# Kernel optimization log

Measured on AMD Instinct MI355X. Metric: run time of the kernel, lower is better.

The kernel has to match this reference:

```python
import jax, jax.numpy as jnp
import numpy as np

B, SEQ, S, DIM_IN, DIM_K, DIM_V = 4, 2048, 128, 512, 64, 64
L = SEQ + 2 * S
NEG = -1e30  # stand-in for log(0) in the tril mask (finite for stable vjp)


def _layernorm(x, g, b, eps=1e-5):
    m = jnp.mean(x, axis=-1, keepdims=True)
    v = jnp.var(x, axis=-1, keepdims=True)
    return (x - m) / jnp.sqrt(v + eps) * g + b


def setup_inputs() -> dict:
    key = jax.random.key(0)
    ks = jax.random.split(key, 18)
    w = lambda k, shape, s=0.02: (jax.random.normal(k, shape, jnp.float32) * s)
    inp = {
        "x": jax.random.normal(ks[0], (B, L, DIM_IN), jnp.float32),
        "Wq": w(ks[1], (DIM_IN, DIM_K)),
        "Wk": w(ks[2], (DIM_IN, DIM_K)),
        "Wv": w(ks[3], (DIM_IN, DIM_V)),
        "Wq_s": w(ks[4], (DIM_IN, DIM_K)),
        "Wk_s": w(ks[5], (DIM_IN, DIM_K)),
        "Wv_s": w(ks[6], (DIM_IN, DIM_V)),
        "Wq_e": w(ks[7], (DIM_IN, DIM_K)),
        "Wk_e": w(ks[8], (DIM_IN, DIM_K)),
        "Wv_e": w(ks[9], (DIM_IN, DIM_V)),
        "ln_g": jnp.ones((DIM_IN,), jnp.float32),
        "ln_b": jnp.zeros((DIM_IN,), jnp.float32),
        "ln_s_g": jnp.ones((DIM_IN,), jnp.float32),
        "ln_s_b": jnp.zeros((DIM_IN,), jnp.float32),
        "ln_e_g": jnp.ones((DIM_IN,), jnp.float32),
        "ln_e_b": jnp.zeros((DIM_IN,), jnp.float32),
        "cope_emb": jax.random.normal(ks[10], (DIM_K, S), jnp.float32),
        "offset": 0,
    }
    return inp


def reference(x, Wq, Wk, Wv, Wq_s, Wk_s, Wv_s, Wq_e, Wk_e, Wv_e,
              ln_g, ln_b, ln_s_g, ln_s_b, ln_e_g, ln_e_b, cope_emb, offset):
    # extract_state: first/last state_len tokens
    xs, xm, xe = x[:, :S], x[:, S:L - S], x[:, -S:]
    xm = _layernorm(xm, ln_g, ln_b)
    xs = _layernorm(xs, ln_s_g, ln_s_b)
    xe = _layernorm(xe, ln_e_g, ln_e_b)

    q, k, v = xm @ Wq, xm @ Wk, xm @ Wv          # (B, SEQ, dk/dv)
    q_s, k_s, v_s = xs @ Wq_s, xs @ Wk_s, xs @ Wv_s
    q_e, k_e, v_e = xe @ Wq_e, xe @ Wk_e, xe @ Wv_e

    # CoPE bias over the non-state block
    logits = jnp.einsum('bqd,bkd->bqk', q, k)    # (B, SEQ, SEQ)
    gates = jax.nn.sigmoid(logits)
    pos = jnp.flip(jnp.cumsum(jnp.flip(gates, -1), axis=-1), -1)
    pos = jnp.minimum(pos, jnp.float32(S - 1))
    pos_ceil = jnp.ceil(pos).astype(jnp.int32)
    pos_floor = jnp.floor(pos).astype(jnp.int32)
    logits_int = jnp.einsum('bqd,dk->bqk', q, cope_emb)  # (B, SEQ, S)
    logits_c = jnp.take_along_axis(logits_int, pos_ceil, axis=-1)
    logits_f = jnp.take_along_axis(logits_int, pos_floor, axis=-1)
    wfrac = pos - pos_floor.astype(pos.dtype)
    bias = logits_c * wfrac + logits_f * (1.0 - wfrac)   # (B, SEQ, SEQ)

    q_full = jnp.concatenate([q_s, q, q_e], axis=1)      # (B, L, dk)
    k_full = jnp.concatenate([k_s, k, k_e], axis=1)
    v_full = jnp.concatenate([v_s, v, v_e], axis=1)

    # explicit tril log-mask bias with CoPE injected in the middle block
    tri = jnp.tril(jnp.ones((L, L), dtype=bool))
    attn_bias = jnp.where(tri, 0.0, NEG).astype(jnp.float32)
    attn_bias = jnp.broadcast_to(attn_bias, (B, L, L))
    attn_bias = attn_bias.at[:, S:L - S, S:L - S].add(bias)

    scale = 1.0 / jnp.sqrt(jnp.float32(DIM_K))
    scores = jnp.einsum('bqd,bkd->bqk', q_full, k_full) * scale + attn_bias
    att = jax.nn.softmax(scores, axis=-1)
    return jnp.einsum('bqk,bkd->bqd', att, v_full)       # (B, L, dv)
```

## Files before the change

kernel.cpp:

```cpp
#include <hip/hip_runtime.h>
#include <math.h>

#define B_    4
#define SEQ_  2048
#define S_    128
#define L_    2304
#define DIN   512
#define DK    64
#define NEGINF (-1e30f)
#define SCALE 0.125f
#define NCOLS 2176
#define NMID  8192
#define NEDGE 1024
#define LE    2304
#define PROWS 4352
#define PEPITCH 4608

typedef _Float16 f16;
typedef __attribute__((ext_vector_type(8))) _Float16 half8;
typedef __attribute__((ext_vector_type(4))) float f32x4;

union U4 { uint4 u; f16 h[8]; };

__global__ __launch_bounds__(256) void k_ln(
    const float* __restrict__ x,
    const float* __restrict__ g0, const float* __restrict__ b0,
    const float* __restrict__ gs, const float* __restrict__ bs,
    const float* __restrict__ ge, const float* __restrict__ be,
    f16* __restrict__ xh, f16* __restrict__ xl)
{
    const int wave = threadIdx.x >> 6, lane = threadIdx.x & 63;
    const int row  = blockIdx.x * 4 + wave;
    const float4* xr = (const float4*)(x + (size_t)row * DIN);
    float4 v0 = xr[lane], v1 = xr[lane + 64];
    float s  = v0.x + v0.y + v0.z + v0.w + v1.x + v1.y + v1.z + v1.w;
    float s2 = v0.x*v0.x + v0.y*v0.y + v0.z*v0.z + v0.w*v0.w
             + v1.x*v1.x + v1.y*v1.y + v1.z*v1.z + v1.w*v1.w;
    #pragma unroll
    for (int m = 1; m < 64; m <<= 1) { s += __shfl_xor(s, m); s2 += __shfl_xor(s2, m); }
    float mean = s * (1.f / DIN);
    float var  = s2 * (1.f / DIN) - mean * mean;
    float rstd = rsqrtf(var + 1e-5f);

    const int r = row % L_;
    const float *gg, *bb;
    if (r < S_)            { gg = gs; bb = bs; }
    else if (r >= L_ - S_) { gg = ge; bb = be; }
    else                   { gg = g0; bb = b0; }
    float4 ga = ((const float4*)gg)[lane], gb = ((const float4*)gg)[lane + 64];
    float4 ba = ((const float4*)bb)[lane], bb4 = ((const float4*)bb)[lane + 64];

    float n0[4], n1[4];
    n0[0] = (v0.x - mean) * rstd * ga.x + ba.x;
    n0[1] = (v0.y - mean) * rstd * ga.y + ba.y;
    n0[2] = (v0.z - mean) * rstd * ga.z + ba.z;
    n0[3] = (v0.w - mean) * rstd * ga.w + ba.w;
    n1[0] = (v1.x - mean) * rstd * gb.x + bb4.x;
    n1[1] = (v1.y - mean) * rstd * gb.y + bb4.y;
    n1[2] = (v1.z - mean) * rstd * gb.z + bb4.z;
    n1[3] = (v1.w - mean) * rstd * gb.w + bb4.w;

    union { uint2 u; f16 h[4]; } h0, h1, l0, l1;
    #pragma unroll
    for (int i = 0; i < 4; ++i) {
        h0.h[i] = (f16)n0[i]; l0.h[i] = (f16)(n0[i] - (float)h0.h[i]);
        h1.h[i] = (f16)n1[i]; l1.h[i] = (f16)(n1[i] - (float)h1.h[i]);
    }
    f16* ph = xh + (size_t)row * DIN;
    f16* pl = xl + (size_t)row * DIN;
    *(uint2*)(ph + 4 * lane)       = h0.u;
    *(uint2*)(ph + 256 + 4 * lane) = h1.u;
    *(uint2*)(pl + 4 * lane)       = l0.u;
    *(uint2*)(pl + 256 + 4 * lane) = l1.u;
}

__global__ __launch_bounds__(256) void k_proj(
    const f16* __restrict__ xh, const f16* __restrict__ xl,
    const float* __restrict__ Wq,  const float* __restrict__ Wk,  const float* __restrict__ Wv,
    const float* __restrict__ Wqs, const float* __restrict__ Wks, const float* __restrict__ Wvs,
    const float* __restrict__ Wqe, const float* __restrict__ Wke, const float* __restrict__ Wve,
    float* __restrict__ qf, float* __restrict__ kf, float* __restrict__ vf,
    f16* __restrict__ qsp, f16* __restrict__ ksp, f16* __restrict__ vhT)
{
    __shared__ f16 As[64 * 136];
    __shared__ f16 Bs[64 * 136];
    const int tid  = threadIdx.x;
    const int row0 = blockIdx.x * 64;
    const int rseq = row0 % L_;
    const int seg  = (rseq < S_) ? 0 : (rseq >= L_ - S_) ? 2 : 1;
    const int m    = blockIdx.y;
    const float* W;
    float* outf;
    if (m == 0)      { W = (seg == 0) ? Wqs : (seg == 2) ? Wqe : Wq; outf = qf; }
    else if (m == 1) { W = (seg == 0) ? Wks : (seg == 2) ? Wke : Wk; outf = kf; }
    else             { W = (seg == 0) ? Wvs : (seg == 2) ? Wve : Wv; outf = vf; }

    const int w = tid >> 6, lane = tid & 63;
    const int cl = lane & 15, quad = lane >> 4;
    const int r0 = 32 * (w >> 1), c0 = 32 * (w & 1);

    f32x4 acc[2][2];
    #pragma unroll
    for (int i = 0; i < 2; ++i)
        #pragma unroll
        for (int j = 0; j < 2; ++j) acc[i][j] = 0.f;

    for (int kc = 0; kc < DIN; kc += 64) {
        __syncthreads();
        #pragma unroll
        for (int i = 0; i < 2; ++i) {
            int g = tid + 256 * i;
            int r = g >> 3, c = g & 7;
            *(uint4*)(As + r * 136 + c * 8) =
                *(const uint4*)(xh + (size_t)(row0 + r) * DIN + kc + c * 8);
            *(uint4*)(As + r * 136 + 64 + c * 8) =
                *(const uint4*)(xl + (size_t)(row0 + r) * DIN + kc + c * 8);
        }
        #pragma unroll
        for (int i = 0; i < 4; ++i) {
            int g = tid + 256 * i;
            int k = g >> 4, c4 = g & 15;
            float4 wv = ((const float4*)W)[(size_t)(kc + k) * 16 + c4];
            f16 h0 = (f16)wv.x, h1 = (f16)wv.y, h2 = (f16)wv.z, h3 = (f16)wv.w;
            Bs[(c4 * 4 + 0) * 136 + k] = h0;
            Bs[(c4 * 4 + 1) * 136 + k] = h1;
            Bs[(c4 * 4 + 2) * 136 + k] = h2;
            Bs[(c4 * 4 + 3) * 136 + k] = h3;
            Bs[(c4 * 4 + 0) * 136 + 64 + k] = (f16)(wv.x - (float)h0);
            Bs[(c4 * 4 + 1) * 136 + 64 + k] = (f16)(wv.y - (float)h1);
            Bs[(c4 * 4 + 2) * 136 + 64 + k] = (f16)(wv.z - (float)h2);
            Bs[(c4 * 4 + 3) * 136 + 64 + k] = (f16)(wv.w - (float)h3);
// ... 28 lines not shown
    }

    const int bI = row0 / L_;
    const int rb = row0 - bI * L_;
    f16* sp = (m == 0) ? qsp : ksp;
    #pragma unroll
    for (int rs = 0; rs < 2; ++rs)
        #pragma unroll
        for (int cs = 0; cs < 2; ++cs)
            #pragma unroll
            for (int r = 0; r < 4; ++r) {
                int lrow = r0 + 16 * rs + quad * 4 + r;
                int col  = c0 + 16 * cs + cl;
                float v  = acc[rs][cs][r];
                size_t grow = (size_t)(row0 + lrow);
                outf[grow * DK + col] = v;
                if (m < 2) {
                    f16 hv = (f16)v;
                    sp[grow * 128 + col]      = hv;
                    sp[grow * 128 + 64 + col] = (f16)(v - (float)hv);
                } else {
                    vhT[(size_t)(bI * 64 + col) * L_ + rb + lrow] = (f16)v;
                }
            }
}

__global__ __launch_bounds__(256) void k_dots(
    const f16* __restrict__ qsp, const f16* __restrict__ ksp,
    float* __restrict__ D, float* __restrict__ G)
{
    __shared__ f16 Qs[128 * 136];
    __shared__ f16 Ks[64 * 136];
    const int tid  = threadIdx.x;
    const int gr0  = blockIdx.x * 128;
    const int by   = blockIdx.y;
    const int col0 = by * 64;
    const int b    = gr0 >> 11;
    const int q0   = gr0 & 2047;
    const size_t qrow0 = (size_t)b * L_ + S_ + q0;
    const size_t krow0 = (size_t)b * L_ + col0;

    #pragma unroll
    for (int i = 0; i < 8; ++i) {
        int g = tid + 256 * i;
        int r = g >> 4, c = g & 15;
        *(uint4*)(Qs + r * 136 + c * 8) = *(const uint4*)(qsp + (qrow0 + r) * 128 + c * 8);
    }
    #pragma unroll
    for (int i = 0; i < 4; ++i) {
        int g = tid + 256 * i;
        int r = g >> 4, c = g & 15;
        *(uint4*)(Ks + r * 136 + c * 8) = *(const uint4*)(ksp + (krow0 + r) * 128 + c * 8);
    }
    __syncthreads();

// ... 19 lines not shown
        for (int c = 0; c < 4; ++c) {
            const f16* base = Ks + (16 * c + cl) * 136 + h * 32 + quad * 8;
            bh[c] = *(const half8*)(base);
            bl[c] = *(const half8*)(base + 64);
        }
        #pragma unroll
        for (int rs = 0; rs < 2; ++rs)
            #pragma unroll
            for (int c = 0; c < 4; ++c) {
                acc[rs][c] = __builtin_amdgcn_mfma_f32_16x16x32_f16(ah[rs], bh[c], acc[rs][c], 0, 0, 0);
                acc[rs][c] = __builtin_amdgcn_mfma_f32_16x16x32_f16(ah[rs], bl[c], acc[rs][c], 0, 0, 0);
                acc[rs][c] = __builtin_amdgcn_mfma_f32_16x16x32_f16(al[rs], bh[c], acc[rs][c], 0, 0, 0);
            }
    }

    const bool writeD = (by < 2) || ((by - 2) <= (q0 >> 6) + 1);
    if (writeD) {
        #pragma unroll
        for (int rs = 0; rs < 2; ++rs)
            #pragma unroll
            for (int c = 0; c < 4; ++c)
                #pragma unroll
                for (int r = 0; r < 4; ++r) {
                    int mrow = gr0 + 32 * w + 16 * rs + quad * 4 + r;
                    int n    = col0 + 16 * c + cl;
                    D[(size_t)mrow * NCOLS + n] = acc[rs][c][r];
                }
    }
    if (by >= 2) {
        const int chm = by - 2;
        #pragma unroll
        for (int rs = 0; rs < 2; ++rs)
            #pragma unroll
            for (int r = 0; r < 4; ++r) {
                float s = 0.f;
                #pragma unroll
                for (int c = 0; c < 4; ++c)
                    s += 1.f / (1.f + __expf(-acc[rs][c][r]));
                #pragma unroll
                for (int off = 1; off < 16; off <<= 1) s += __shfl_xor(s, off);
                if (cl == 0)
                    G[(size_t)(gr0 + 32 * w + 16 * rs + quad * 4 + r) * 32 + chm] = s;
            }
    }
}

__global__ __launch_bounds__(256) void k_scan(
    const float* __restrict__ qf, const float* __restrict__ cope,
    const float* __restrict__ G, float* __restrict__ D)
{
    __shared__ float qv[DK];
    __shared__ float li[128];
    __shared__ float red[256];
    __shared__ float wtot[4];
    __shared__ float Gs[32];
    const int tid = threadIdx.x;
    const int gr  = blockIdx.x;
    const int b   = gr >> 11;
    const int q   = gr & 2047;
    const size_t grow = (size_t)b * L_ + S_ + q;
    const int qlim = (q & ~63) + 64;

    if (tid < 16) ((float4*)qv)[tid] = ((const float4*)qf)[grow * 16 + tid];
    if (tid >= 16 && tid < 24) ((float4*)Gs)[tid - 16] = ((const float4*)G)[(size_t)gr * 8 + tid - 16];
    __syncthreads();
    if (tid < 128) {
        float a = 0.f;
        #pragma unroll
        for (int d = 0; d < DK; ++d) a += qv[d] * cope[d * S_ + tid];
        li[tid] = a;
    }

    const float* Dr = D + (size_t)gr * NCOLS;
    const int j0 = tid * 8;
    float dot[8], gte[8];
    float csum = 0.f;
    if (j0 < qlim) {
        *(float4*)&dot[0] = *(const float4*)(Dr + 128 + j0);
        *(float4*)&dot[4] = *(const float4*)(Dr + 128 + j0 + 4);
        #pragma unroll
        for (int jj = 0; jj < 8; ++jj) {
            gte[jj] = 1.f / (1.f + __expf(-dot[jj]));
            csum += gte[jj];
        }
    } else {
        #pragma unroll
        for (int jj = 0; jj < 8; ++jj) { dot[jj] = 0.f; gte[jj] = 0.f; }
    }
    float sv = (tid < 128) ? Dr[tid] * SCALE : NEGINF;

    const int lane = tid & 63, wid = tid >> 6;
    float inc = csum;
    #pragma unroll
    for (int off = 1; off < 64; off <<= 1) {
        float u = __shfl_down(inc, off, 64);
        if (lane + off < 64) inc += u;
    }
    if (lane == 0) wtot[wid] = inc;
    __syncthreads();
    float wsuf = 0.f;
    #pragma unroll
    for (int w = 0; w < 4; ++w) if (w > wid) wsuf += wtot[w];
    float tail = 0.f;
    for (int c = (q >> 6) + 1; c < 32; ++c) tail += Gs[c];
    float run = inc - csum + wsuf + tail;

    float p8[8];
    #pragma unroll
    for (int jj = 7; jj >= 0; --jj) {
        run += gte[jj];
        float pos = fminf(run, (float)(S_ - 1));
        float pfl = floorf(pos);
        int ic  = (int)ceilf(pos);
        int ifl = (int)pfl;
        float w = pos - pfl;
        float bias = li[ic] * w + li[ifl] * (1.f - w);
        p8[jj] = (j0 + jj <= q) ? dot[jj] * SCALE + bias : NEGINF;
    }

    float mx = sv;
    #pragma unroll
    for (int jj = 0; jj < 8; ++jj) mx = fmaxf(mx, p8[jj]);
    red[tid] = mx;
    __syncthreads();
    for (int off = 128; off > 0; off >>= 1) {
        if (tid < off) red[tid] = fmaxf(red[tid], red[tid + off]);
        __syncthreads();
    }
    mx = red[0];
    __syncthreads();

    float lsum = 0.f;
    float e8[8];
    #pragma unroll
    for (int jj = 0; jj < 8; ++jj) {
        e8[jj] = __expf(p8[jj] - mx);
        lsum += e8[jj];
    }
    float es = 0.f;
    if (tid < 128) { es = __expf(sv - mx); lsum += es; }
    red[tid] = lsum;
    __syncthreads();
    for (int off = 128; off > 0; off >>= 1) {
        if (tid < off) red[tid] += red[tid + off];
        __syncthreads();
    }
    float inv = 1.f / red[0];

    f16* pb = (f16*)D + (size_t)gr * PROWS;
    if (j0 < qlim) {
        U4 o;
        #pragma unroll
        for (int jj = 0; jj < 8; ++jj) o.h[jj] = (f16)(e8[jj] * inv);
        *(uint4*)(pb + 128 + j0) = o.u;
    }
    if (tid < 128) pb[tid] = (f16)(es * inv);
}

__global__ __launch_bounds__(256) void k_pv(
    const f16* __restrict__ Pb, const f16* __restrict__ vhT,
    float* __restrict__ Opart)
{
    __shared__ f16 Ps[64 * 72];
    __shared__ f16 Vt[64 * 72];
    const int tid = threadIdx.x;
    const int gr0 = blockIdx.x * 64;
    const int ks  = blockIdx.y;
    const int b   = gr0 >> 11, q0 = gr0 & 2047;
    const int cmax  = (191 + q0) >> 6;
    const int c_beg = ks * 9;
    int c_end = c_beg + 9;
    if (c_end > 34) c_end = 34;
    if (c_end > cmax + 1) c_end = cmax + 1;

    const int w = tid >> 6, lane = tid & 63;
    const int cl = lane & 15, quad = lane >> 4;
    f32x4 acc[4];
    #pragma unroll
    for (int c = 0; c < 4; ++c) acc[c] = 0.f;

    for (int ch = c_beg; ch < c_end; ++ch) {
        __syncthreads();
        #pragma unroll
        for (int i = 0; i < 2; ++i) {
            int g = tid + 256 * i;
            int r = g >> 3, c = g & 7;
            *(uint4*)(Ps + r * 72 + c * 8) =
                *(const uint4*)(Pb + (size_t)(gr0 + r) * PROWS + ch * 64 + c * 8);
            *(uint4*)(Vt + r * 72 + c * 8) =
                *(const uint4*)(vhT + (size_t)(b * 64 + r) * L_ + ch * 64 + c * 8);
        }
        __syncthreads();
        #pragma unroll
        for (int h = 0; h < 2; ++h) {
            half8 a = *(const half8*)(Ps + (16 * w + cl) * 72 + h * 32 + quad * 8);
            #pragma unroll
            for (int c = 0; c < 4; ++c) {
                half8 bv = *(const half8*)(Vt + (16 * c + cl) * 72 + h * 32 + quad * 8);
                acc[c] = __builtin_amdgcn_mfma_f32_16x16x32_f16(a, bv, acc[c], 0, 0, 0);
            }
        }
    }
    #pragma unroll
    for (int c = 0; c < 4; ++c)
        #pragma unroll
        for (int r = 0; r < 4; ++r) {
            int mrow = gr0 + 16 * w + quad * 4 + r;
            int n    = 16 * c + cl;
            Opart[((size_t)ks * NMID + mrow) * DK + n] = acc[c][r];
        }
}

__global__ __launch_bounds__(256) void k_merge(
    const float* __restrict__ Opart, float* __restrict__ out)
{
    const int e  = blockIdx.x * 256 + threadIdx.x;
    const int gr = e >> 6, c = e & 63;
    const int b  = gr >> 11, q = gr & 2047;
    const int NP = NMID * DK;
    float s = Opart[e] + Opart[e + NP] + Opart[e + 2 * NP] + Opart[e + 3 * NP];
    out[((size_t)b * L_ + S_ + q) * DK + c] = s;
}

__global__ __launch_bounds__(256) void k_dots_edge(
    const f16* __restrict__ qsp, const f16* __restrict__ ksp,
    float* __restrict__ De)
{
    const int bx   = blockIdx.x;
    const int b    = bx >> 1;
    const int half = bx & 1;
    const int by   = blockIdx.y;
    if (half == 0 && by > 1) return;

    __shared__ f16 Qs[128 * 136];
    __shared__ f16 Ks[64 * 136];
    const int tid = threadIdx.x;
    const int er0 = bx * 128;
    const size_t qrow0 = (size_t)b * L_ + (half ? 2176 : 0);
    const size_t krow0 = (size_t)b * L_ + by * 64;

    #pragma unroll
    for (int i = 0; i < 8; ++i) {
        int g = tid + 256 * i;
        int r = g >> 4, c = g & 15;
        *(uint4*)(Qs + r * 136 + c * 8) = *(const uint4*)(qsp + (qrow0 + r) * 128 + c * 8);
    }
    #pragma unroll
    for (int i = 0; i < 4; ++i) {
        int g = tid + 256 * i;
        int r = g >> 4, c = g & 15;
        *(uint4*)(Ks + r * 136 + c * 8) = *(const uint4*)(ksp + (krow0 + r) * 128 + c * 8);
    }
    __syncthreads();

    const int w = tid >> 6, lane = tid & 63;
    const int cl = lane & 15, quad = lane >> 4;

    f32x4 acc[2][4];
    #pragma unroll
    for (int i = 0; i < 2; ++i)
        #pragma unroll
        for (int j = 0; j < 4; ++j) acc[i][j] = 0.f;

    #pragma unroll
    for (int h = 0; h < 2; ++h) {
        half8 ah[2], al[2], bh[4], bl[4];
        #pragma unroll
        for (int rs = 0; rs < 2; ++rs) {
            const f16* base = Qs + (32 * w + 16 * rs + cl) * 136 + h * 32 + quad * 8;
            ah[rs] = *(const half8*)(base);
            al[rs] = *(const half8*)(base + 64);
        }
        #pragma unroll
        for (int c = 0; c < 4; ++c) {
            const f16* base = Ks + (16 * c + cl) * 136 + h * 32 + quad * 8;
            bh[c] = *(const half8*)(base);
            bl[c] = *(const half8*)(base + 64);
        }
        #pragma unroll
        for (int rs = 0; rs < 2; ++rs)
            #pragma unroll
            for (int c = 0; c < 4; ++c) {
                acc[rs][c] = __builtin_amdgcn_mfma_f32_16x16x32_f16(ah[rs], bh[c], acc[rs][c], 0, 0, 0);
                acc[rs][c] = __builtin_amdgcn_mfma_f32_16x16x32_f16(ah[rs], bl[c], acc[rs][c], 0, 0, 0);
                acc[rs][c] = __builtin_amdgcn_mfma_f32_16x16x32_f16(al[rs], bh[c], acc[rs][c], 0, 0, 0);
            }
    }

    #pragma unroll
    for (int rs = 0; rs < 2; ++rs)
        #pragma unroll
        for (int c = 0; c < 4; ++c)
            #pragma unroll
            for (int r = 0; r < 4; ++r) {
                int erow = er0 + 32 * w + 16 * rs + quad * 4 + r;
                int n    = by * 64 + 16 * c + cl;
                De[(size_t)erow * LE + n] = acc[rs][c][r];
            }
}

__global__ __launch_bounds__(256) void k_soft_edge(float* __restrict__ De)
{
    __shared__ float red[256];
    const int tid = threadIdx.x;
    const int er  = blockIdx.x;
    const int r   = er & 255;
    const int Q   = (r < 128) ? r : (2048 + r);
    const size_t rowoff = (size_t)er * LE;

    float v[9];
    #pragma unroll
    for (int i = 0; i < 9; ++i) {
        int j = tid + 256 * i;
        float d = De[rowoff + j];
        v[i] = (j <= Q) ? d * SCALE : NEGINF;
    }
    float mx = v[0];
    #pragma unroll
    for (int i = 1; i < 9; ++i) mx = fmaxf(mx, v[i]);
    red[tid] = mx;
    __syncthreads();
    for (int off = 128; off > 0; off >>= 1) {
        if (tid < off) red[tid] = fmaxf(red[tid], red[tid + off]);
        __syncthreads();
    }
    mx = red[0];
    __syncthreads();

    float lsum = 0.f;
    #pragma unroll
    for (int i = 0; i < 9; ++i) {
        v[i] = __expf(v[i] - mx);
        lsum += v[i];
    }
    red[tid] = lsum;
    __syncthreads();
    for (int off = 128; off > 0; off >>= 1) {
        if (tid < off) red[tid] += red[tid + off];
        __syncthreads();
    }
    float inv = 1.f / red[0];
    f16* pe = (f16*)De + (size_t)er * PEPITCH;
    #pragma unroll
    for (int i = 0; i < 9; ++i)
        pe[tid + 256 * i] = (f16)(v[i] * inv);
}

__global__ __launch_bounds__(256) void k_pv_edge(
    const f16* __restrict__ Pe, const f16* __restrict__ vhT,
    float* __restrict__ Oe)
{
    __shared__ f16 Ps[64 * 72];
    __shared__ f16 Vt[64 * 72];
    const int tid = threadIdx.x;
    const int er0 = blockIdx.x * 64;
    const int ks  = blockIdx.y;
    const int b   = er0 >> 8, r0 = er0 & 255;
    const int Qmax = (r0 < 128) ? (r0 + 63) : (2048 + r0 + 63);
    const int cmax = Qmax >> 6;
    const int c_beg = ks * 5;
    int c_end = c_beg + 5;
    if (c_end > 36) c_end = 36;
    if (c_end > cmax + 1) c_end = cmax + 1;

    const int w = tid >> 6, lane = tid & 63;
    const int cl = lane & 15, quad = lane >> 4;
    f32x4 acc[4];
    #pragma unroll
    for (int c = 0; c < 4; ++c) acc[c] = 0.f;

    for (int ch = c_beg; ch < c_end; ++ch) {
        __syncthreads();
        #pragma unroll
        for (int i = 0; i < 2; ++i) {
            int g = tid + 256 * i;
            int r = g >> 3, c = g & 7;
            *(uint4*)(Ps + r * 72 + c * 8) =
                *(const uint4*)(Pe + (size_t)(er0 + r) * PEPITCH + ch * 64 + c * 8);
            *(uint4*)(Vt + r * 72 + c * 8) =
                *(const uint4*)(vhT + (size_t)(b * 64 + r) * L_ + ch * 64 + c * 8);
        }
        __syncthreads();
        #pragma unroll
        for (int h = 0; h < 2; ++h) {
            half8 a = *(const half8*)(Ps + (16 * w + cl) * 72 + h * 32 + quad * 8);
            #pragma unroll
            for (int c = 0; c < 4; ++c) {
                half8 bv = *(const half8*)(Vt + (16 * c + cl) * 72 + h * 32 + quad * 8);
                acc[c] = __builtin_amdgcn_mfma_f32_16x16x32_f16(a, bv, acc[c], 0, 0, 0);
            }
        }
    }
    #pragma unroll
    for (int c = 0; c < 4; ++c)
        #pragma unroll
        for (int r = 0; r < 4; ++r) {
            int erow = er0 + 16 * w + quad * 4 + r;
            int n    = 16 * c + cl;
            Oe[((size_t)ks * NEDGE + erow) * DK + n] = acc[c][r];
        }
}

__global__ __launch_bounds__(256) void k_merge_edge(
    const float* __restrict__ Oe, float* __restrict__ out)
{
    const int e  = blockIdx.x * 256 + threadIdx.x;
    const int er = e >> 6, c = e & 63;
    const int b  = er >> 8, r = er & 255;
    const int gQ = (r < 128) ? r : (2048 + r);
    const int NP = NEDGE * DK;
    float s = 0.f;
    #pragma unroll
    for (int i = 0; i < 8; ++i) s += Oe[e + i * NP];
    out[((size_t)b * L_ + gQ) * DK + c] = s;
}

extern "C" void kernel_launch(void* const* d_in, const int* in_sizes, int n_in,
                              void* d_out, int out_size, void* d_ws, size_t ws_size,
                              hipStream_t stream)
{
    const float* x    = (const float*)d_in[0];
    const float* Wq   = (const float*)d_in[1];
    const float* Wk   = (const float*)d_in[2];
    const float* Wv   = (const float*)d_in[3];
    const float* Wqs  = (const float*)d_in[4];
    const float* Wks  = (const float*)d_in[5];
    const float* Wvs  = (const float*)d_in[6];
    const float* Wqe  = (const float*)d_in[7];
    const float* Wke  = (const float*)d_in[8];
    const float* Wve  = (const float*)d_in[9];
    const float* g0   = (const float*)d_in[10];
    const float* b0   = (const float*)d_in[11];
    const float* gs   = (const float*)d_in[12];
    const float* bs   = (const float*)d_in[13];
    const float* ge   = (const float*)d_in[14];
    const float* be   = (const float*)d_in[15];
    const float* cope = (const float*)d_in[16];

    const size_t NR = (size_t)B_ * L_;
    float* ws = (float*)d_ws;
    float* qf    = ws;
    float* kf    = qf + NR * DK;
    float* vf    = kf + NR * DK;
    float* Opart = vf + NR * DK;
    float* G     = Opart + (size_t)4 * NMID * DK;
    f16*   qsp   = (f16*)(G + (size_t)NMID * 32);
    f16*   ksp   = qsp + NR * 128;
    f16*   vhT   = ksp + NR * 128;
    float* D     = (float*)(vhT + NR * DK);
    f16*   xh    = (f16*)D;
    f16*   xl    = xh + NR * DIN;
    float* De    = D;
    float* Oe    = Opart;
    float* out   = (float*)d_out;

    k_ln  <<<L_ * B_ / 4, 256, 0, stream>>>(x, g0, b0, gs, bs, ge, be, xh, xl);
    k_proj<<<dim3(144, 3), 256, 0, stream>>>(xh, xl, Wq, Wk, Wv, Wqs, Wks, Wvs,
                                             Wqe, Wke, Wve, qf, kf, vf,
                                             qsp, ksp, vhT);
    k_dots<<<dim3(NMID / 128, 34), 256, 0, stream>>>(qsp, ksp, D, G);
    k_scan<<<NMID, 256, 0, stream>>>(qf, cope, G, D);
    k_pv  <<<dim3(NMID / 64, 4), 256, 0, stream>>>((const f16*)D, vhT, Opart);
    k_merge<<<NMID * DK / 256, 256, 0, stream>>>(Opart, out);
    k_dots_edge<<<dim3(8, 36), 256, 0, stream>>>(qsp, ksp, De);
    k_soft_edge<<<NEDGE, 256, 0, stream>>>(De);
    k_pv_edge<<<dim3(NEDGE / 64, 8), 256, 0, stream>>>((const f16*)De, vhT, Oe);
    k_merge_edge<<<NEDGE * DK / 256, 256, 0, stream>>>(Oe, out);
}
```

Baseline: 223.2 us.

## Fuse layernorm into projection and merge edge-path kernels into main-path kernels

Layernorm is folded into the projection kernel: per-row statistics are computed in shared memory and the hi/lo f16 split happens while A tiles are staged, which removes the separate LN pass and its f16 round-trip through memory. The edge-row dots, softmax, PV and merge kernels are combined with their middle-block counterparts by widening grids and branching on block index, so ten launches become five. The fp32 q/k/v outputs are dropped, and CoPE logits are now rebuilt from the split f16 q. The cost is some extra reads of x and gamma/beta per projection block, plus idle early-exit blocks in the combined dots grid.

```diff
diff --git a/kernel.cpp b/kernel.cpp
--- a/kernel.cpp
+++ b/kernel.cpp
@@ -22,78 +22,49 @@
 
 union U4 { uint4 u; f16 h[8]; };
 
-__global__ __launch_bounds__(256) void k_ln(
+__global__ __launch_bounds__(256) void k_proj(
     const float* __restrict__ x,
+    const float* __restrict__ Wq,  const float* __restrict__ Wk,  const float* __restrict__ Wv,
+    const float* __restrict__ Wqs, const float* __restrict__ Wks, const float* __restrict__ Wvs,
+    const float* __restrict__ Wqe, const float* __restrict__ Wke, const float* __restrict__ Wve,
     const float* __restrict__ g0, const float* __restrict__ b0,
     const float* __restrict__ gs, const float* __restrict__ bs,
     const float* __restrict__ ge, const float* __restrict__ be,
-    f16* __restrict__ xh, f16* __restrict__ xl)
-{
-    const int wave = threadIdx.x >> 6, lane = threadIdx.x & 63;
-    const int row  = blockIdx.x * 4 + wave;
-    const float4* xr = (const float4*)(x + (size_t)row * DIN);
-    float4 v0 = xr[lane], v1 = xr[lane + 64];
-    float s  = v0.x + v0.y + v0.z + v0.w + v1.x + v1.y + v1.z + v1.w;
-    float s2 = v0.x*v0.x + v0.y*v0.y + v0.z*v0.z + v0.w*v0.w
-             + v1.x*v1.x + v1.y*v1.y + v1.z*v1.z + v1.w*v1.w;
-    #pragma unroll
-    for (int m = 1; m < 64; m <<= 1) { s += __shfl_xor(s, m); s2 += __shfl_xor(s2, m); }
-    float mean = s * (1.f / DIN);
-    float var  = s2 * (1.f / DIN) - mean * mean;
-    float rstd = rsqrtf(var + 1e-5f);
-
-    const int r = row % L_;
-    const float *gg, *bb;
-    if (r < S_)            { gg = gs; bb = bs; }
-    else if (r >= L_ - S_) { gg = ge; bb = be; }
-    else                   { gg = g0; bb = b0; }
-    float4 ga = ((const float4*)gg)[lane], gb = ((const float4*)gg)[lane + 64];
-    float4 ba = ((const float4*)bb)[lane], bb4 = ((const float4*)bb)[lane + 64];
-
-    float n0[4], n1[4];
-    n0[0] = (v0.x - mean) * rstd * ga.x + ba.x;
-    n0[1] = (v0.y - mean) * rstd * ga.y + ba.y;
-    n0[2] = (v0.z - mean) * rstd * ga.z + ba.z;
-    n0[3] = (v0.w - mean) * rstd * ga.w + ba.w;
-    n1[0] = (v1.x - mean) * rstd * gb.x + bb4.x;
-    n1[1] = (v1.y - mean) * rstd * gb.y + bb4.y;
-    n1[2] = (v1.z - mean) * rstd * gb.z + bb4.z;
-    n1[3] = (v1.w - mean) * rstd * gb.w + bb4.w;
-
-    union { uint2 u; f16 h[4]; } h0, h1, l0, l1;
-    #pragma unroll
-    for (int i = 0; i < 4; ++i) {
-        h0.h[i] = (f16)n0[i]; l0.h[i] = (f16)(n0[i] - (float)h0.h[i]);
-        h1.h[i] = (f16)n1[i]; l1.h[i] = (f16)(n1[i] - (float)h1.h[i]);
-    }
-    f16* ph = xh + (size_t)row * DIN;
-    f16* pl = xl + (size_t)row * DIN;
-    *(uint2*)(ph + 4 * lane)       = h0.u;
-    *(uint2*)(ph + 256 + 4 * lane) = h1.u;
-    *(uint2*)(pl + 4 * lane)       = l0.u;
-    *(uint2*)(pl + 256 + 4 * lane) = l1.u;
-}
-
-__global__ __launch_bounds__(256) void k_proj(
-    const f16* __restrict__ xh, const f16* __restrict__ xl,
-    const float* __restrict__ Wq,  const float* __restrict__ Wk,  const float* __restrict__ Wv,
-    const float* __restrict__ Wqs, const float* __restrict__ Wks, const float* __restrict__ Wvs,
-    const float* __restrict__ Wqe, const float* __restrict__ Wke, const float* __restrict__ Wve,
-    float* __restrict__ qf, float* __restrict__ kf, float* __restrict__ vf,
     f16* __restrict__ qsp, f16* __restrict__ ksp, f16* __restrict__ vhT)
 {
     __shared__ f16 As[64 * 136];
     __shared__ f16 Bs[64 * 136];
+    __shared__ float mean_s[64], rstd_s[64];
     const int tid  = threadIdx.x;
     const int row0 = blockIdx.x * 64;
     const int rseq = row0 % L_;
     const int seg  = (rseq < S_) ? 0 : (rseq >= L_ - S_) ? 2 : 1;
     const int m    = blockIdx.y;
     const float* W;
-    float* outf;
-    if (m == 0)      { W = (seg == 0) ? Wqs : (seg == 2) ? Wqe : Wq; outf = qf; }
-    else if (m == 1) { W = (seg == 0) ? Wks : (seg == 2) ? Wke : Wk; outf = kf; }
-    else             { W = (seg == 0) ? Wvs : (seg == 2) ? Wve : Wv; outf = vf; }
+    if (m == 0)      W = (seg == 0) ? Wqs : (seg == 2) ? Wqe : Wq;
+    else if (m == 1) W = (seg == 0) ? Wks : (seg == 2) ? Wke : Wk;
+    else             W = (seg == 0) ? Wvs : (seg == 2) ? Wve : Wv;
+    const float* gg = (seg == 0) ? gs : (seg == 2) ? ge : g0;
+    const float* bb = (seg == 0) ? bs : (seg == 2) ? be : b0;
+
+    {
+        const int rr = tid >> 2, qq = tid & 3;
+        const float4* xr = (const float4*)(x + (size_t)(row0 + rr) * DIN) + qq * 32;
+        float s = 0.f, s2 = 0.f;
+        #pragma unroll
+        for (int i = 0; i < 32; ++i) {
+            float4 v = xr[i];
+            s  += v.x + v.y + v.z + v.w;
+            s2 += v.x * v.x + v.y * v.y + v.z * v.z + v.w * v.w;
+        }
+        s  += __shfl_xor(s, 1);  s  += __shfl_xor(s, 2);
+        s2 += __shfl_xor(s2, 1); s2 += __shfl_xor(s2, 2);
+        if (qq == 0) {
+            float mean = s * (1.f / DIN);
+            mean_s[rr] = mean;
+            rstd_s[rr] = rsqrtf(s2 * (1.f / DIN) - mean * mean + 1e-5f);
+        }
+    }
 
     const int w = tid >> 6, lane = tid & 63;
     const int cl = lane & 15, quad = lane >> 4;
@@ -110,11 +81,32 @@
         #pragma unroll
         for (int i = 0; i < 2; ++i) {
             int g = tid + 256 * i;
-            int r = g >> 3, c = g & 7;
-            *(uint4*)(As + r * 136 + c * 8) =
-                *(const uint4*)(xh + (size_t)(row0 + r) * DIN + kc + c * 8);
-            *(uint4*)(As + r * 136 + 64 + c * 8) =
-                *(const uint4*)(xl + (size_t)(row0 + r) * DIN + kc + c * 8);
+            int r = g >> 3, c8 = g & 7;
+            const float* xp = x + (size_t)(row0 + r) * DIN + kc + c8 * 8;
+            float4 a0 = *(const float4*)xp;
+            float4 a1 = *(const float4*)(xp + 4);
+            float4 gA = *(const float4*)(gg + kc + c8 * 8);
+            float4 gB = *(const float4*)(gg + kc + c8 * 8 + 4);
+            float4 bA = *(const float4*)(bb + kc + c8 * 8);
+            float4 bB = *(const float4*)(bb + kc + c8 * 8 + 4);
+            float mean = mean_s[r], rstd = rstd_s[r];
+            float n[8];
+            n[0] = (a0.x - mean) * rstd * gA.x + bA.x;
+            n[1] = (a0.y - mean) * rstd * gA.y + bA.y;
+            n[2] = (a0.z - mean) * rstd * gA.z + bA.z;
+            n[3] = (a0.w - mean) * rstd * gA.w + bA.w;
+            n[4] = (a1.x - mean) * rstd * gB.x + bB.x;
+            n[5] = (a1.y - mean) * rstd * gB.y + bB.y;
+            n[6] = (a1.z - mean) * rstd * gB.z + bB.z;
+            n[7] = (a1.w - mean) * rstd * gB.w + bB.w;
+            U4 hi, lo;
+            #pragma unroll
+            for (int j = 0; j < 8; ++j) {
+                hi.h[j] = (f16)n[j];
+                lo.h[j] = (f16)(n[j] - (float)hi.h[j]);
+            }
+            *(uint4*)(As + r * 136 + c8 * 8)      = hi.u;
+            *(uint4*)(As + r * 136 + 64 + c8 * 8) = lo.u;
         }
         #pragma unroll
         for (int i = 0; i < 4; ++i) {
@@ -173,7 +165,6 @@
                 int col  = c0 + 16 * cs + cl;
                 float v  = acc[rs][cs][r];
                 size_t grow = (size_t)(row0 + lrow);
-                outf[grow * DK + col] = v;
                 if (m < 2) {
                     f16 hv = (f16)v;
                     sp[grow * 128 + col]      = hv;
@@ -186,18 +177,30 @@
 
 __global__ __launch_bounds__(256) void k_dots(
     const f16* __restrict__ qsp, const f16* __restrict__ ksp,
-    float* __restrict__ D, float* __restrict__ G)
+    float* __restrict__ D, float* __restrict__ G, float* __restrict__ De)
 {
+    const int bx = blockIdx.x, by = blockIdx.y;
+    const bool edge = (bx >= 64);
+    int b, q0 = 0;
+    size_t qrow0;
+    if (!edge) {
+        if (by >= 34) return;
+        b = bx >> 4;
+        q0 = (bx * 128) & 2047;
+        qrow0 = (size_t)b * L_ + S_ + q0;
+    } else {
+        int ex = bx - 64;
+        b = ex >> 1;
+        int half = ex & 1;
+        if (half == 0 && by > 1) return;
+        qrow0 = (size_t)b * L_ + (half ? 2176 : 0);
+    }
+    const int col0 = by * 64;
+    const size_t krow0 = (size_t)b * L_ + col0;
+
     __shared__ f16 Qs[128 * 136];
     __shared__ f16 Ks[64 * 136];
-    const int tid  = threadIdx.x;
-    const int gr0  = blockIdx.x * 128;
-    const int by   = blockIdx.y;
-    const int col0 = by * 64;
-    const int b    = gr0 >> 11;
-    const int q0   = gr0 & 2047;
-    const size_t qrow0 = (size_t)b * L_ + S_ + q0;
-    const size_t krow0 = (size_t)b * L_ + col0;
+    const int tid = threadIdx.x;
 
     #pragma unroll
     for (int i = 0; i < 8; ++i) {
@@ -247,163 +250,236 @@
             }
     }
 
-    const bool writeD = (by < 2) || ((by - 2) <= (q0 >> 6) + 1);
-    if (writeD) {
+    if (!edge) {
+        const int gr0 = bx * 128;
+        const bool writeD = (by < 2) || ((by - 2) <= (q0 >> 6) + 1);
+        if (writeD) {
+            #pragma unroll
+            for (int rs = 0; rs < 2; ++rs)
+                #pragma unroll
+                for (int c = 0; c < 4; ++c)
+                    #pragma unroll
+                    for (int r = 0; r < 4; ++r) {
+                        int mrow = gr0 + 32 * w + 16 * rs + quad * 4 + r;
+                        int n    = col0 + 16 * c + cl;
+                        D[(size_t)mrow * NCOLS + n] = acc[rs][c][r];
+                    }
+        }
+        if (by >= 2) {
+            const int chm = by - 2;
+            #pragma unroll
+            for (int rs = 0; rs < 2; ++rs)
+                #pragma unroll
+                for (int r = 0; r < 4; ++r) {
+                    float s = 0.f;
+                    #pragma unroll
+                    for (int c = 0; c < 4; ++c)
+                        s += 1.f / (1.f + __expf(-acc[rs][c][r]));
+                    #pragma unroll
+                    for (int off = 1; off < 16; off <<= 1) s += __shfl_xor(s, off);
+                    if (cl == 0)
+                        G[(size_t)(gr0 + 32 * w + 16 * rs + quad * 4 + r) * 32 + chm] = s;
+                }
+        }
+    } else {
+        const int er0 = (bx - 64) * 128;
         #pragma unroll
         for (int rs = 0; rs < 2; ++rs)
             #pragma unroll
             for (int c = 0; c < 4; ++c)
                 #pragma unroll
                 for (int r = 0; r < 4; ++r) {
-                    int mrow = gr0 + 32 * w + 16 * rs + quad * 4 + r;
+                    int erow = er0 + 32 * w + 16 * rs + quad * 4 + r;
                     int n    = col0 + 16 * c + cl;
-                    D[(size_t)mrow * NCOLS + n] = acc[rs][c][r];
+                    De[(size_t)erow * LE + n] = acc[rs][c][r];
                 }
     }
-    if (by >= 2) {
-        const int chm = by - 2;
-        #pragma unroll
-        for (int rs = 0; rs < 2; ++rs)
-            #pragma unroll
-            for (int r = 0; r < 4; ++r) {
-                float s = 0.f;
-                #pragma unroll
-                for (int c = 0; c < 4; ++c)
-                    s += 1.f / (1.f + __expf(-acc[rs][c][r]));
-                #pragma unroll
-                for (int off = 1; off < 16; off <<= 1) s += __shfl_xor(s, off);
-                if (cl == 0)
-                    G[(size_t)(gr0 + 32 * w + 16 * rs + quad * 4 + r) * 32 + chm] = s;
-            }
-    }
 }
 
 __global__ __launch_bounds__(256) void k_scan(
-    const float* __restrict__ qf, const float* __restrict__ cope,
-    const float* __restrict__ G, float* __restrict__ D)
+    const f16* __restrict__ qsp, const float* __restrict__ cope,
+    const float* __restrict__ G, float* __restrict__ D, float* __restrict__ De)
 {
-    __shared__ float qv[DK];
+    __shared__ f16   qvh[128];
     __shared__ float li[128];
-    __shared__ float red[256];
-    __shared__ float wtot[4];
     __shared__ float Gs[32];
+    __shared__ float wtot[4], wmax[4], wsum[4];
     const int tid = threadIdx.x;
     const int gr  = blockIdx.x;
-    const int b   = gr >> 11;
-    const int q   = gr & 2047;
-    const size_t grow = (size_t)b * L_ + S_ + q;
-    const int qlim = (q & ~63) + 64;
-
-    if (tid < 16) ((float4*)qv)[tid] = ((const float4*)qf)[grow * 16 + tid];
-    if (tid >= 16 && tid < 24) ((float4*)Gs)[tid - 16] = ((const float4*)G)[(size_t)gr * 8 + tid - 16];
-    __syncthreads();
-    if (tid < 128) {
-        float a = 0.f;
-        #pragma unroll
-        for (int d = 0; d < DK; ++d) a += qv[d] * cope[d * S_ + tid];
-        li[tid] = a;
-    }
-
-    const float* Dr = D + (size_t)gr * NCOLS;
-    const int j0 = tid * 8;
-    float dot[8], gte[8];
-    float csum = 0.f;
-    if (j0 < qlim) {
-        *(float4*)&dot[0] = *(const float4*)(Dr + 128 + j0);
-        *(float4*)&dot[4] = *(const float4*)(Dr + 128 + j0 + 4);
+    const int lane = tid & 63, wid = tid >> 6;
+
+    if (gr < NMID) {
+        const int b = gr >> 11;
+        const int q = gr & 2047;
+        const size_t grow = (size_t)b * L_ + S_ + q;
+        const int qlim = (q & ~63) + 64;
+
+        if (tid < 16) ((uint4*)qvh)[tid] = ((const uint4*)(qsp + grow * 128))[tid];
+        if (tid >= 16 && tid < 24)
+            ((float4*)Gs)[tid - 16] = ((const float4*)G)[(size_t)gr * 8 + tid - 16];
+        __syncthreads();
+        if (tid < 128) {
+            float a = 0.f;
+            #pragma unroll
+            for (int d = 0; d < DK; ++d)
+                a += ((float)qvh[d] + (float)qvh[64 + d]) * cope[d * S_ + tid];
+            li[tid] = a;
+        }
+
+        const float* Dr = D + (size_t)gr * NCOLS;
+        const int j0 = tid * 8;
+        float dot[8], gte[8];
+        float csum = 0.f;
+        if (j0 < qlim) {
+            *(float4*)&dot[0] = *(const float4*)(Dr + 128 + j0);
+            *(float4*)&dot[4] = *(const float4*)(Dr + 128 + j0 + 4);
+            #pragma unroll
+            for (int jj = 0; jj < 8; ++jj) {
+                gte[jj] = 1.f / (1.f + __expf(-dot[jj]));
+                csum += gte[jj];
+            }
+        } else {
+            #pragma unroll
+            for (int jj = 0; jj < 8; ++jj) { dot[jj] = 0.f; gte[jj] = 0.f; }
+        }
+        float sv = (tid < 128) ? Dr[tid] * SCALE : NEGINF;
+
+        float inc = csum;
+        #pragma unroll
+        for (int off = 1; off < 64; off <<= 1) {
+            float u = __shfl_down(inc, off, 64);
+            if (lane + off < 64) inc += u;
+        }
+        if (lane == 0) wtot[wid] = inc;
+        __syncthreads();
+        float wsuf = 0.f;
+        #pragma unroll
+        for (int w = 0; w < 4; ++w) if (w > wid) wsuf += wtot[w];
+        float tail = 0.f;
+        for (int c = (q >> 6) + 1; c < 32; ++c) tail += Gs[c];
+        float run = inc - csum + wsuf + tail;
+
+        float p8[8];
+        #pragma unroll
+        for (int jj = 7; jj >= 0; --jj) {
+            run += gte[jj];
+            float pos = fminf(run, (float)(S_ - 1));
+            float pfl = floorf(pos);
+            int ic  = (int)ceilf(pos);
+            int ifl = (int)pfl;
+            float w = pos - pfl;
+            float bias = li[ic] * w + li[ifl] * (1.f - w);
+            p8[jj] = (j0 + jj <= q) ? dot[jj] * SCALE + bias : NEGINF;
+        }
+
+        float mx = sv;
+        #pragma unroll
+        for (int jj = 0; jj < 8; ++jj) mx = fmaxf(mx, p8[jj]);
+        #pragma unroll
+        for (int off = 1; off < 64; off <<= 1) mx = fmaxf(mx, __shfl_xor(mx, off));
+        if (lane == 0) wmax[wid] = mx;
+        __syncthreads();
+        mx = fmaxf(fmaxf(wmax[0], wmax[1]), fmaxf(wmax[2], wmax[3]));
+
+        float lsum = 0.f;
+        float e8[8];
         #pragma unroll
         for (int jj = 0; jj < 8; ++jj) {
-            gte[jj] = 1.f / (1.f + __expf(-dot[jj]));
-            csum += gte[jj];
-        }
+            e8[jj] = __expf(p8[jj] - mx);
+            lsum += e8[jj];
+        }
+        float es = 0.f;
+        if (tid < 128) { es = __expf(sv - mx); lsum += es; }
+        #pragma unroll
+        for (int off = 1; off < 64; off <<= 1) lsum += __shfl_xor(lsum, off);
+        if (lane == 0) wsum[wid] = lsum;
+        __syncthreads();
+        float inv = 1.f / (wsum[0] + wsum[1] + wsum[2] + wsum[3]);
+
+        f16* pb = (f16*)D + (size_t)gr * PROWS;
+        if (j0 < qlim) {
+            U4 o;
+            #pragma unroll
+            for (int jj = 0; jj < 8; ++jj) o.h[jj] = (f16)(e8[jj] * inv);
+            *(uint4*)(pb + 128 + j0) = o.u;
+        }
+        if (tid < 128) pb[tid] = (f16)(es * inv);
     } else {
-        #pragma unroll
-        for (int jj = 0; jj < 8; ++jj) { dot[jj] = 0.f; gte[jj] = 0.f; }
-    }
-    float sv = (tid < 128) ? Dr[tid] * SCALE : NEGINF;
-
-    const int lane = tid & 63, wid = tid >> 6;
-    float inc = csum;
-    #pragma unroll
-    for (int off = 1; off < 64; off <<= 1) {
-        float u = __shfl_down(inc, off, 64);
-        if (lane + off < 64) inc += u;
-    }
-    if (lane == 0) wtot[wid] = inc;
-    __syncthreads();
-    float wsuf = 0.f;
-    #pragma unroll
-    for (int w = 0; w < 4; ++w) if (w > wid) wsuf += wtot[w];
-    float tail = 0.f;
-    for (int c = (q >> 6) + 1; c < 32; ++c) tail += Gs[c];
-    float run = inc - csum + wsuf + tail;
-
-    float p8[8];
-    #pragma unroll
-    for (int jj = 7; jj >= 0; --jj) {
-        run += gte[jj];
-        float pos = fminf(run, (float)(S_ - 1));
-        float pfl = floorf(pos);
-        int ic  = (int)ceilf(pos);
-        int ifl = (int)pfl;
-        float w = pos - pfl;
-        float bias = li[ic] * w + li[ifl] * (1.f - w);
-        p8[jj] = (j0 + jj <= q) ? dot[jj] * SCALE + bias : NEGINF;
-    }
-
-    float mx = sv;
-    #pragma unroll
-    for (int jj = 0; jj < 8; ++jj) mx = fmaxf(mx, p8[jj]);
-    red[tid] = mx;
-    __syncthreads();
-    for (int off = 128; off > 0; off >>= 1) {
-        if (tid < off) red[tid] = fmaxf(red[tid], red[tid + off]);
-        __syncthreads();
-    }
-    mx = red[0];
-    __syncthreads();
-
-    float lsum = 0.f;
-    float e8[8];
-    #pragma unroll
-    for (int jj = 0; jj < 8; ++jj) {
-        e8[jj] = __expf(p8[jj] - mx);
-        lsum += e8[jj];
-    }
-    float es = 0.f;
-    if (tid < 128) { es = __expf(sv - mx); lsum += es; }
-    red[tid] = lsum;
-    __syncthreads();
-    for (int off = 128; off > 0; off >>= 1) {
-        if (tid < off) red[tid] += red[tid + off];
-        __syncthreads();
-    }
-    float inv = 1.f / red[0];
-
-    f16* pb = (f16*)D + (size_t)gr * PROWS;
-    if (j0 < qlim) {
-        U4 o;
-        #pragma unroll
-        for (int jj = 0; jj < 8; ++jj) o.h[jj] = (f16)(e8[jj] * inv);
-        *(uint4*)(pb + 128 + j0) = o.u;
-    }
-    if (tid < 128) pb[tid] = (f16)(es * inv);
+        const int er = gr - NMID;
+        const int r  = er & 255;
+        const int Q  = (r < 128) ? r : (2048 + r);
+        const size_t rowoff = (size_t)er * LE;
+
+        float v[9];
+        #pragma unroll
+        for (int i = 0; i < 9; ++i) {
+            int j = tid + 256 * i;
+            float d = De[rowoff + j];
+            v[i] = (j <= Q) ? d * SCALE : NEGINF;
+        }
+        float mx = v[0];
+        #pragma unroll
+        for (int i = 1; i < 9; ++i) mx = fmaxf(mx, v[i]);
+        #pragma unroll
+        for (int off = 1; off < 64; off <<= 1) mx = fmaxf(mx, __shfl_xor(mx, off));
+        if (lane == 0) wmax[wid] = mx;
+        __syncthreads();
+        mx = fmaxf(fmaxf(wmax[0], wmax[1]), fmaxf(wmax[2], wmax[3]));
+
+        float lsum = 0.f;
+        #pragma unroll
+        for (int i = 0; i < 9; ++i) {
+            v[i] = __expf(v[i] - mx);
+            lsum += v[i];
+        }
+        #pragma unroll
+        for (int off = 1; off < 64; off <<= 1) lsum += __shfl_xor(lsum, off);
+        if (lane == 0) wsum[wid] = lsum;
+        __syncthreads();
+        float inv = 1.f / (wsum[0] + wsum[1] + wsum[2] + wsum[3]);
+
+        f16* pe = (f16*)De + (size_t)er * PEPITCH;
+        #pragma unroll
+        for (int i = 0; i < 9; ++i)
+            pe[tid + 256 * i] = (f16)(v[i] * inv);
+    }
 }
 
 __global__ __launch_bounds__(256) void k_pv(
-    const f16* __restrict__ Pb, const f16* __restrict__ vhT,
-    float* __restrict__ Opart)
+    const f16* __restrict__ Pmid, const f16* __restrict__ Pedge,
+    const f16* __restrict__ vhT,
+    float* __restrict__ Opart, float* __restrict__ Oe)
 {
     __shared__ f16 Ps[64 * 72];
     __shared__ f16 Vt[64 * 72];
     const int tid = threadIdx.x;
-    const int gr0 = blockIdx.x * 64;
+    const int bx  = blockIdx.x;
     const int ks  = blockIdx.y;
-    const int b   = gr0 >> 11, q0 = gr0 & 2047;
-    const int cmax  = (191 + q0) >> 6;
+    const bool edge = (bx >= 128);
+
+    const f16* Pb;
+    size_t pitch;
+    int row0, b, cap, cmax;
+    float* outp;
+    if (!edge) {
+        row0 = bx * 64;
+        b = row0 >> 11;
+        int q0 = row0 & 2047;
+        Pb = Pmid; pitch = PROWS; cap = 34;
+        cmax = (191 + q0) >> 6;
+        outp = Opart + (size_t)ks * NMID * DK;
+    } else {
+        row0 = (bx - 128) * 64;
+        b = row0 >> 8;
+        int r0 = row0 & 255;
+        Pb = Pedge; pitch = PEPITCH; cap = 36;
+        int Qmax = (r0 < 128) ? (r0 + 63) : (2048 + r0 + 63);
+        cmax = Qmax >> 6;
+        outp = Oe + (size_t)ks * NEDGE * DK;
+    }
     const int c_beg = ks * 9;
     int c_end = c_beg + 9;
-    if (c_end > 34) c_end = 34;
+    if (c_end > cap) c_end = cap;
     if (c_end > cmax + 1) c_end = cmax + 1;
 
     const int w = tid >> 6, lane = tid & 63;
@@ -419,7 +495,7 @@
             int g = tid + 256 * i;
             int r = g >> 3, c = g & 7;
             *(uint4*)(Ps + r * 72 + c * 8) =
-                *(const uint4*)(Pb + (size_t)(gr0 + r) * PROWS + ch * 64 + c * 8);
+                *(const uint4*)(Pb + (size_t)(row0 + r) * pitch + ch * 64 + c * 8);
             *(uint4*)(Vt + r * 72 + c * 8) =
                 *(const uint4*)(vhT + (size_t)(b * 64 + r) * L_ + ch * 64 + c * 8);
         }
@@ -438,214 +514,32 @@
     for (int c = 0; c < 4; ++c)
         #pragma unroll
         for (int r = 0; r < 4; ++r) {
-            int mrow = gr0 + 16 * w + quad * 4 + r;
+            int mrow = row0 + 16 * w + quad * 4 + r;
             int n    = 16 * c + cl;
-            Opart[((size_t)ks * NMID + mrow) * DK + n] = acc[c][r];
+            outp[(size_t)mrow * DK + n] = acc[c][r];
         }
 }
 
 __global__ __launch_bounds__(256) void k_merge(
-    const float* __restrict__ Opart, float* __restrict__ out)
+    const float* __restrict__ Opart, const float* __restrict__ Oe,
+    float* __restrict__ out)
 {
-    const int e  = blockIdx.x * 256 + threadIdx.x;
-    const int gr = e >> 6, c = e & 63;
-    const int b  = gr >> 11, q = gr & 2047;
-    const int NP = NMID * DK;
-    float s = Opart[e] + Opart[e + NP] + Opart[e + 2 * NP] + Opart[e + 3 * NP];
-    out[((size_t)b * L_ + S_ + q) * DK + c] = s;
-}
-
-__global__ __launch_bounds__(256) void k_dots_edge(
-    const f16* __restrict__ qsp, const f16* __restrict__ ksp,
-    float* __restrict__ De)
-{
-    const int bx   = blockIdx.x;
-    const int b    = bx >> 1;
-    const int half = bx & 1;
-    const int by   = blockIdx.y;
-    if (half == 0 && by > 1) return;
-
-    __shared__ f16 Qs[128 * 136];
-    __shared__ f16 Ks[64 * 136];
-    const int tid = threadIdx.x;
-    const int er0 = bx * 128;
-    const size_t qrow0 = (size_t)b * L_ + (half ? 2176 : 0);
-    const size_t krow0 = (size_t)b * L_ + by * 64;
-
-    #pragma unroll
-    for (int i = 0; i < 8; ++i) {
-        int g = tid + 256 * i;
-        int r = g >> 4, c = g & 15;
-        *(uint4*)(Qs + r * 136 + c * 8) = *(const uint4*)(qsp + (qrow0 + r) * 128 + c * 8);
-    }
-    #pragma unroll
-    for (int i = 0; i < 4; ++i) {
-        int g = tid + 256 * i;
-        int r = g >> 4, c = g & 15;
-        *(uint4*)(Ks + r * 136 + c * 8) = *(const uint4*)(ksp + (krow0 + r) * 128 + c * 8);
-    }
-    __syncthreads();
-
-    const int w = tid >> 6, lane = tid & 63;
-    const int cl = lane & 15, quad = lane >> 4;
-
-    f32x4 acc[2][4];
-    #pragma unroll
-    for (int i = 0; i < 2; ++i)
-        #pragma unroll
-        for (int j = 0; j < 4; ++j) acc[i][j] = 0.f;
-
-    #pragma unroll
-    for (int h = 0; h < 2; ++h) {
-        half8 ah[2], al[2], bh[4], bl[4];
-        #pragma unroll
-        for (int rs = 0; rs < 2; ++rs) {
-            const f16* base = Qs + (32 * w + 16 * rs + cl) * 136 + h * 32 + quad * 8;
-            ah[rs] = *(const half8*)(base);
-            al[rs] = *(const half8*)(base + 64);
-        }
-        #pragma unroll
-        for (int c = 0; c < 4; ++c) {
-            const f16* base = Ks + (16 * c + cl) * 136 + h * 32 + quad * 8;
-            bh[c] = *(const half8*)(base);
-            bl[c] = *(const half8*)(base + 64);
-        }
-        #pragma unroll
-        for (int rs = 0; rs < 2; ++rs)
-            #pragma unroll
-            for (int c = 0; c < 4; ++c) {
-                acc[rs][c] = __builtin_amdgcn_mfma_f32_16x16x32_f16(ah[rs], bh[c], acc[rs][c], 0, 0, 0);
-                acc[rs][c] = __builtin_amdgcn_mfma_f32_16x16x32_f16(ah[rs], bl[c], acc[rs][c], 0, 0, 0);
-                acc[rs][c] = __builtin_amdgcn_mfma_f32_16x16x32_f16(al[rs], bh[c], acc[rs][c], 0, 0, 0);
-            }
-    }
-
-    #pragma unroll
-    for (int rs = 0; rs < 2; ++rs)
-        #pragma unroll
-        for (int c = 0; c < 4; ++c)
-            #pragma unroll
-            for (int r = 0; r < 4; ++r) {
-                int erow = er0 + 32 * w + 16 * rs + quad * 4 + r;
-                int n    = by * 64 + 16 * c + cl;
-                De[(size_t)erow * LE + n] = acc[rs][c][r];
-            }
-}
-
-__global__ __launch_bounds__(256) void k_soft_edge(float* __restrict__ De)
-{
-    __shared__ float red[256];
-    const int tid = threadIdx.x;
-    const int er  = blockIdx.x;
-    const int r   = er & 255;
-    const int Q   = (r < 128) ? r : (2048 + r);
-    const size_t rowoff = (size_t)er * LE;
-
-    float v[9];
-    #pragma unroll
-    for (int i = 0; i < 9; ++i) {
-        int j = tid + 256 * i;
-        float d = De[rowoff + j];
-        v[i] = (j <= Q) ? d * SCALE : NEGINF;
-    }
-    float mx = v[0];
-    #pragma unroll
-    for (int i = 1; i < 9; ++i) mx = fmaxf(mx, v[i]);
-    red[tid] = mx;
-    __syncthreads();
-    for (int off = 128; off > 0; off >>= 1) {
-        if (tid < off) red[tid] = fmaxf(red[tid], red[tid + off]);
-        __syncthreads();
-    }
-    mx = red[0];
-    __syncthreads();
-
-    float lsum = 0.f;
-    #pragma unroll
-    for (int i = 0; i < 9; ++i) {
-        v[i] = __expf(v[i] - mx);
-        lsum += v[i];
-    }
-    red[tid] = lsum;
-    __syncthreads();
-    for (int off = 128; off > 0; off >>= 1) {
-        if (tid < off) red[tid] += red[tid + off];
-        __syncthreads();
-    }
-    float inv = 1.f / red[0];
-    f16* pe = (f16*)De + (size_t)er * PEPITCH;
-    #pragma unroll
-    for (int i = 0; i < 9; ++i)
-        pe[tid + 256 * i] = (f16)(v[i] * inv);
-}
-
-__global__ __launch_bounds__(256) void k_pv_edge(
-    const f16* __restrict__ Pe, const f16* __restrict__ vhT,
-    float* __restrict__ Oe)
-{
-    __shared__ f16 Ps[64 * 72];
-    __shared__ f16 Vt[64 * 72];
-    const int tid = threadIdx.x;
-    const int er0 = blockIdx.x * 64;
-    const int ks  = blockIdx.y;
-    const int b   = er0 >> 8, r0 = er0 & 255;
-    const int Qmax = (r0 < 128) ? (r0 + 63) : (2048 + r0 + 63);
-    const int cmax = Qmax >> 6;
-    const int c_beg = ks * 5;
-    int c_end = c_beg + 5;
-    if (c_end > 36) c_end = 36;
-    if (c_end > cmax + 1) c_end = cmax + 1;
-
-    const int w = tid >> 6, lane = tid & 63;
-    const int cl = lane & 15, quad = lane >> 4;
-    f32x4 acc[4];
-    #pragma unroll
-    for (int c = 0; c < 4; ++c) acc[c] = 0.f;
-
-    for (int ch = c_beg; ch < c_end; ++ch) {
-        __syncthreads();
-        #pragma unroll
-        for (int i = 0; i < 2; ++i) {
-            int g = tid + 256 * i;
-            int r = g >> 3, c = g & 7;
-            *(uint4*)(Ps + r * 72 + c * 8) =
-                *(const uint4*)(Pe + (size_t)(er0 + r) * PEPITCH + ch * 64 + c * 8);
-            *(uint4*)(Vt + r * 72 + c * 8) =
-                *(const uint4*)(vhT + (size_t)(b * 64 + r) * L_ + ch * 64 + c * 8);
-        }
-        __syncthreads();
-        #pragma unroll
-        for (int h = 0; h < 2; ++h) {
-            half8 a = *(const half8*)(Ps + (16 * w + cl) * 72 + h * 32 + quad * 8);
-            #pragma unroll
-            for (int c = 0; c < 4; ++c) {
-                half8 bv = *(const half8*)(Vt + (16 * c + cl) * 72 + h * 32 + quad * 8);
-                acc[c] = __builtin_amdgcn_mfma_f32_16x16x32_f16(a, bv, acc[c], 0, 0, 0);
-            }
-        }
-    }
-    #pragma unroll
-    for (int c = 0; c < 4; ++c)
-        #pragma unroll
-        for (int r = 0; r < 4; ++r) {
-            int erow = er0 + 16 * w + quad * 4 + r;
-            int n    = 16 * c + cl;
-            Oe[((size_t)ks * NEDGE + erow) * DK + n] = acc[c][r];
-        }
-}
-
-__global__ __launch_bounds__(256) void k_merge_edge(
-    const float* __restrict__ Oe, float* __restrict__ out)
-{
-    const int e  = blockIdx.x * 256 + threadIdx.x;
-    const int er = e >> 6, c = e & 63;
-    const int b  = er >> 8, r = er & 255;
-    const int gQ = (r < 128) ? r : (2048 + r);
-    const int NP = NEDGE * DK;
-    float s = 0.f;
-    #pragma unroll
-    for (int i = 0; i < 8; ++i) s += Oe[e + i * NP];
-    out[((size_t)b * L_ + gQ) * DK + c] = s;
+    const int e = blockIdx.x * 256 + threadIdx.x;
+    if (e < NMID * DK) {
+        const int gr = e >> 6, c = e & 63;
+        const int b  = gr >> 11, q = gr & 2047;
+        const int NP = NMID * DK;
+        float s = Opart[e] + Opart[e + NP] + Opart[e + 2 * NP] + Opart[e + 3 * NP];
+        out[((size_t)b * L_ + S_ + q) * DK + c] = s;
+    } else {
+        const int e2 = e - NMID * DK;
+        const int er = e2 >> 6, c = e2 & 63;
+        const int b  = er >> 8, r = er & 255;
+        const int gQ = (r < 128) ? r : (2048 + r);
+        const int NP = NEDGE * DK;
+        float s = Oe[e2] + Oe[e2 + NP] + Oe[e2 + 2 * NP] + Oe[e2 + 3 * NP];
+        out[((size_t)b * L_ + gQ) * DK + c] = s;
+    }
 }
 
 extern "C" void kernel_launch(void* const* d_in, const int* in_sizes, int n_in,
@@ -671,32 +565,22 @@
     const float* cope = (const float*)d_in[16];
 
     const size_t NR = (size_t)B_ * L_;
-    float* ws = (float*)d_ws;
-    float* qf    = ws;
-    float* kf    = qf + NR * DK;
-    float* vf    = kf + NR * DK;
-    float* Opart = vf + NR * DK;
-    float* G     = Opart + (size_t)4 * NMID * DK;
-    f16*   qsp   = (f16*)(G + (size_t)NMID * 32);
+    f16*   qsp   = (f16*)d_ws;
     f16*   ksp   = qsp + NR * 128;
     f16*   vhT   = ksp + NR * 128;
-    float* D     = (float*)(vhT + NR * DK);
-    f16*   xh    = (f16*)D;
-    f16*   xl    = xh + NR * DIN;
-    float* De    = D;
-    float* Oe    = Opart;
+    float* G     = (float*)(vhT + NR * 64);
+    float* Opart = G + (size_t)NMID * 32;
+    float* Oe    = Opart + (size_t)4 * NMID * DK;
+    float* D     = Oe + (size_t)4 * NEDGE * DK;
+    float* De    = D + (size_t)NMID * NCOLS;
     float* out   = (float*)d_out;
 
-    k_ln  <<<L_ * B_ / 4, 256, 0, stream>>>(x, g0, b0, gs, bs, ge, be, xh, xl);
-    k_proj<<<dim3(144, 3), 256, 0, stream>>>(xh, xl, Wq, Wk, Wv, Wqs, Wks, Wvs,
-                                             Wqe, Wke, Wve, qf, kf, vf,
-                                             qsp, ksp, vhT);
-    k_dots<<<dim3(NMID / 128, 34), 256, 0, stream>>>(qsp, ksp, D, G);
-    k_scan<<<NMID, 256, 0, stream>>>(qf, cope, G, D);
-    k_pv  <<<dim3(NMID / 64, 4), 256, 0, stream>>>((const f16*)D, vhT, Opart);
-    k_merge<<<NMID * DK / 256, 256, 0, stream>>>(Opart, out);
-    k_dots_edge<<<dim3(8, 36), 256, 0, stream>>>(qsp, ksp, De);
-    k_soft_edge<<<NEDGE, 256, 0, stream>>>(De);
-    k_pv_edge<<<dim3(NEDGE / 64, 8), 256, 0, stream>>>((const f16*)De, vhT, Oe);
-    k_merge_edge<<<NEDGE * DK / 256, 256, 0, stream>>>(Oe, out);
+    k_proj<<<dim3(144, 3), 256, 0, stream>>>(x, Wq, Wk, Wv, Wqs, Wks, Wvs,
+                                             Wqe, Wke, Wve, g0, b0, gs, bs,
+                                             ge, be, qsp, ksp, vhT);
+    k_dots<<<dim3(72, 36), 256, 0, stream>>>(qsp, ksp, D, G, De);
+    k_scan<<<NMID + NEDGE, 256, 0, stream>>>(qsp, cope, G, D, De);
+    k_pv  <<<dim3(144, 4), 256, 0, stream>>>((const f16*)D, (const f16*)De,
+                                             vhT, Opart, Oe);
+    k_merge<<<(NMID + NEDGE) * DK / 256, 256, 0, stream>>>(Opart, Oe, out);
 }
```

Measured after the change: 201.7 us. -9.6%, faster.
